# Performance work log

Hardware: AMD Instinct MI355X
Metric: run time of the kernel (lower is better)

The kernel has to match this reference:

```python
import jax, jax.numpy as jnp
import numpy as np

B, N, D = 32, 4096, 256
NC, NTPC, NVPT, NS = 16, 8, 4, 16
NT = NC * NTPC          # 128 type codes
NV = NT * NVPT          # 512 variant codes
THRESH = 0.1            # code_sparsity


def setup_inputs() -> dict:
    key = jax.random.key(0)
    ks = jax.random.split(key, 24)
    rn = lambda k, s, sc=0.02: jax.random.normal(k, s, jnp.float32) * sc
    return {
        "X": jax.random.normal(ks[0], (B, N, D), jnp.float32),
        "positions": jax.random.normal(ks[1], (B, N, D), jnp.float32),
        "mask": jnp.ones((B, N), jnp.bool_),
        "category_codes": rn(ks[2], (NC, D)),
        "type_codes": rn(ks[3], (NT, D)),
        "variant_codes": rn(ks[4], (NV, D)),
        "spatial_codes": rn(ks[5], (NS, D)),
        "log_tau": jnp.zeros((1,), jnp.float32),
        "Wk": rn(ks[6], (D, D)), "bk": jnp.zeros((D,), jnp.float32),
        "Wcat": rn(ks[7], (D, D)), "bcat": jnp.zeros((D,), jnp.float32),
        "Wtype": rn(ks[8], (D, D)), "btype": jnp.zeros((D,), jnp.float32),
        "Wvar": rn(ks[9], (D, D)), "bvar": jnp.zeros((D,), jnp.float32),
        "Wsp": rn(ks[10], (D, D)), "bsp": jnp.zeros((D,), jnp.float32),
        "Wg1": rn(ks[11], (D, 2 * D)), "bg1": jnp.zeros((D,), jnp.float32),
        "Wg2": rn(ks[12], (D, D)), "bg2": jnp.zeros((D,), jnp.float32),
        "Wo": rn(ks[13], (D, D)), "bo": jnp.zeros((D,), jnp.float32),
        "ln_g": jnp.ones((D,), jnp.float32), "ln_b": jnp.zeros((D,), jnp.float32),
        "level_weights": jnp.ones((4,), jnp.float32) / 4.0,
    }


def _sparsify(w, thr):
    w = jnp.where(w > thr, w, 0.0)
    return w / (w.sum(-1, keepdims=True) + 1e-8)


def reference(X, positions, mask, category_codes, type_codes, variant_codes,
              spatial_codes, log_tau, Wk, bk, Wcat, bcat, Wtype, btype,
              Wvar, bvar, Wsp, bsp, Wg1, bg1, Wg2, bg2, Wo, bo, ln_g, ln_b,
              level_weights):
    d = X.shape[-1]
    tau = jnp.clip(jnp.exp(log_tau) + 0.1, 0.1, 2.0)  # (1,)
    mv = jnp.finfo(X.dtype).min / 2
    K = X @ Wk.T + bk  # (B,N,d)

    def level(codes, Wq, bq):
        Q = codes @ Wq.T + bq                                    # (M,d)
        attn = jnp.einsum('md,bnd->bmn', Q, K) / jnp.sqrt(jnp.float32(d))
        attn = jnp.where(mask[:, None, :], attn, mv)
        attn = jnp.clip(attn, -50.0, 50.0)
        G = jnp.nan_to_num(jax.nn.softmax(attn, axis=-1))
        H = jnp.einsum('bmn,bnd->bmd', G, X)                     # (B,M,d)
        w_raw = jnp.linalg.norm(H, axis=-1) / tau                # (B,M)
        return H, w_raw

    # level 0: category
    H_cat, w_cat_raw = level(category_codes, Wcat, bcat)
    w_cat_sparse = _sparsify(jax.nn.softmax(w_cat_raw, -1), THRESH)
    # level 1: type (gated by category)
    H_type, w_type_raw = level(type_codes, Wtype, btype)
    w_type_g = (w_type_raw.reshape(-1, NC, NTPC) * w_cat_sparse[:, :, None]).reshape(-1, NT)
    w_type_sparse = _sparsify(jax.nn.softmax(w_type_g, -1), THRESH / 2)
    # level 2: variant (gated by type)
    H_var, w_var_raw = level(variant_codes, Wvar, bvar)
    w_type_exp = jnp.repeat(w_type_sparse, NVPT, axis=-1)        # (B,NV)
    w_var_sparse = _sparsify(jax.nn.softmax(w_var_raw * w_type_exp, -1), THRESH / 4)
    # spatial (independent)
    H_sp, w_sp_raw = level(spatial_codes, Wsp, bsp)
    w_sp_sparse = _sparsify(jax.nn.softmax(w_sp_raw, -1), THRESH)

    z_cat = jnp.einsum('bm,bmd->bd', w_cat_sparse, H_cat)
    z_type = jnp.einsum('bm,bmd->bd', w_type_sparse, H_type)
    z_var = jnp.einsum('bm,bmd->bd', w_var_sparse, H_var)
    z_sp = jnp.einsum('bm,bmd->bd', w_sp_sparse, H_sp)

    lw = jax.nn.softmax(level_weights)
    z = lw[0] * z_cat + lw[1] * z_type + lw[2] * z_var + lw[3] * z_sp

    # position gate: masked mean-pooled positions -> sigmoid gate
    m = mask.astype(X.dtype)
    pos_pool = (positions * m[:, :, None]).sum(1) / (m.sum(1, keepdims=True) + 1e-8)
    h = jax.nn.gelu(jnp.concatenate([z, pos_pool], -1) @ Wg1.T + bg1, approximate=False)
    gate = jax.nn.sigmoid(h @ Wg2.T + bg2)
    z = z * gate

    # out_proj: Linear + LayerNorm
    y = z @ Wo.T + bo
    mu = y.mean(-1, keepdims=True)
    var = ((y - mu) ** 2).mean(-1, keepdims=True)
    y = (y - mu) / jnp.sqrt(var + 1e-5) * ln_g + ln_b
    return y
```

## Files before the change

### kernel.cpp

```cpp
#include <hip/hip_runtime.h>

typedef unsigned short u16;
typedef short v8s __attribute__((ext_vector_type(8)));
typedef float v4f __attribute__((ext_vector_type(4)));

union U16x8 { uint4 u4; v8s s8; u16 us[8]; };

__device__ __forceinline__ u16 f2bf(float x) {
  unsigned int u = __float_as_uint(x);
  u += 0x7fffu + ((u >> 16) & 1u);
  return (u16)(u >> 16);
}

#define GLOBAL_AS __attribute__((address_space(1)))
#define LDS_AS __attribute__((address_space(3)))
__device__ __forceinline__ void async16(const void* g, void* l) {
  __builtin_amdgcn_global_load_lds((const GLOBAL_AS unsigned int*)g,
                                   (LDS_AS unsigned int*)l, 16, 0, 0);
}

#define BB 32
#define NN 4096
#define DD 256
#define M_TOT 672
#define M_PAD 704
#define MT_PER_B 11

__global__ void kz_zero(float* __restrict__ p, int n) {
  int i = blockIdx.x * 256 + threadIdx.x;
  if (i < n) p[i] = 0.f;
}

__global__ void k0_q(const float* __restrict__ cat, const float* __restrict__ typ,
                     const float* __restrict__ var, const float* __restrict__ spc,
                     const float* __restrict__ Wcat, const float* __restrict__ bcat,
                     const float* __restrict__ Wtype, const float* __restrict__ btype,
                     const float* __restrict__ Wvar, const float* __restrict__ bvar,
                     const float* __restrict__ Wsp, const float* __restrict__ bsp,
                     float* __restrict__ Qall) {
  __shared__ float cl[DD];
  const int m = blockIdx.x, tid = threadIdx.x;
  const float* codes = nullptr; const float* W = nullptr; const float* bia = nullptr; int r = 0;
  if (m < 16)       { codes = cat; r = m;       W = Wcat;  bia = bcat; }
  else if (m < 144) { codes = typ; r = m - 16;  W = Wtype; bia = btype; }
  else if (m < 656) { codes = var; r = m - 144; W = Wvar;  bia = bvar; }
  else if (m < 672) { codes = spc; r = m - 656; W = Wsp;   bia = bsp; }
  cl[tid] = (m < M_TOT) ? codes[r * DD + tid] : 0.f;
  __syncthreads();
  if (m < M_TOT) {
    float acc = bia[tid];
    const float4* w4 = (const float4*)(W + (size_t)tid * DD);
    const float4* c4 = (const float4*)cl;
    #pragma unroll 8
    for (int k = 0; k < 64; ++k) {
      float4 a = c4[k], b = w4[k];
      acc += a.x * b.x + a.y * b.y + a.z * b.z + a.w * b.w;
    }
    Qall[m * DD + tid] = acc;
  } else {
    Qall[m * DD + tid] = 0.f;
  }
}

__global__ void k1_qp(const float* __restrict__ Qall, const float* __restrict__ Wk,
                      const float* __restrict__ bk, u16* __restrict__ Qp,
                      float* __restrict__ qbw) {
  __shared__ float ql[DD];
  __shared__ float red[4];
  const int m = blockIdx.x, tid = threadIdx.x;
  ql[tid] = Qall[m * DD + tid];
  __syncthreads();
  float acc = 0.f;
  for (int j = 0; j < DD; ++j) acc += ql[j] * Wk[(size_t)j * DD + tid];
  Qp[m * DD + tid] = f2bf(acc);
  float p = ql[tid] * bk[tid];
  #pragma unroll
  for (int off = 32; off > 0; off >>= 1) p += __shfl_down(p, off, 64);
  if ((tid & 63) == 0) red[tid >> 6] = p;
  __syncthreads();
  if (tid == 0) qbw[m] = red[0] + red[1] + red[2] + red[3];
}

__global__ void k2_cast(const float* __restrict__ X, u16* __restrict__ Xb,
                        u16* __restrict__ XbT) {
  __shared__ u16 tl[64][72];
  const int n0 = blockIdx.x * 64, d0 = blockIdx.y * 64, b = blockIdx.z;
  const int tid = threadIdx.x;
  const int nl = tid >> 4, d4 = tid & 15;
  #pragma unroll
  for (int rr = 0; rr < 4; ++rr) {
    const int n = n0 + nl + rr * 16;
    float4 v = *(const float4*)(X + ((size_t)b * NN + n) * DD + d0 + d4 * 4);
    ushort4 h;
    h.x = f2bf(v.x); h.y = f2bf(v.y); h.z = f2bf(v.z); h.w = f2bf(v.w);
    *(ushort4*)(Xb + ((size_t)b * NN + n) * DD + d0 +
                (((d4 >> 1) ^ (n & 7)) << 3) + (d4 & 1) * 4) = h;
    *(ushort4*)(&tl[nl + rr * 16][d4 * 4]) = h;
  }
  __syncthreads();
  const int dl = tid >> 4, n4 = tid & 15;
  #pragma unroll
  for (int rr = 0; rr < 4; ++rr) {
    const int d = dl + rr * 16;
    ushort4 h;
    h.x = tl[n4 * 4 + 0][d]; h.y = tl[n4 * 4 + 1][d];
    h.z = tl[n4 * 4 + 2][d]; h.w = tl[n4 * 4 + 3][d];
    *(ushort4*)(XbT + ((size_t)b * DD + d0 + d) * NN + n0 +
                (((n4 >> 1) ^ (dl & 7)) << 3) + (n4 & 1) * 4) = h;
  }
}

__global__ __launch_bounds__(256, 2) void pf_fused(
    const u16* __restrict__ Xb, const u16* __restrict__ XbT,
    const u16* __restrict__ Qp, const float* __restrict__ qbw,
    const unsigned char* __restrict__ mask,
    float* __restrict__ Hws, float* __restrict__ sums, float* __restrict__ nrm) {
  __shared__ u16 sX[64 * 256];
  __shared__ u16 sXT[256 * 64];
  __shared__ u16 sP[64 * 64];

  const int id = blockIdx.x;
  const int orig = (id & 7) * 44 + (id >> 3);
  const int b = orig / MT_PER_B;
  const int m0 = (orig - b * MT_PER_B) * 64;

  const int tid = threadIdx.x;
  const int lane = tid & 63, w = tid >> 6;
  const int q = lane >> 4, c16 = lane & 15;
  const int wmQ = (w >> 1) * 32, wn = (w & 1) * 32;
  const int wd = w * 64;

  v8s aq[2][4][2];
  #pragma unroll
  for (int mi = 0; mi < 2; ++mi) {
    const u16* qrow = Qp + (size_t)(m0 + wmQ + mi * 16 + c16) * DD;
    #pragma unroll
    for (int ks = 0; ks < 4; ++ks)
      #pragma unroll
      for (int kk = 0; kk < 2; ++kk) {
        U16x8 u; u.u4 = *(const uint4*)(qrow + ks * 64 + kk * 32 + q * 8);
        aq[mi][ks][kk] = u.s8;
      }
  }
  float qv[2][4];
  #pragma unroll
  for (int mi = 0; mi < 2; ++mi)
    #pragma unroll
    for (int r = 0; r < 4; ++r)
      qv[mi][r] = qbw[m0 + wmQ + mi * 16 + q * 4 + r];

  v4f hacc[4][4];
  #pragma unroll
  for (int mi = 0; mi < 4; ++mi)
    #pragma unroll
    for (int di = 0; di < 4; ++di) hacc[mi][di] = (v4f){0.f, 0.f, 0.f, 0.f};
  float rs[2][4];
  #pragma unroll
  for (int mi = 0; mi < 2; ++mi)
    #pragma unroll
    for (int r = 0; r < 4; ++r) rs[mi][r] = 0.f;

  const u16* XbB = Xb + (size_t)b * NN * DD;
  const u16* XTB = XbT + (size_t)b * DD * NN;
  const unsigned char* mkB = mask + (size_t)b * NN;

  for (int it = 0; it < 64; ++it) {
    const int n0g = it * 64;
    __syncthreads();
    #pragma unroll
    for (int i = 0; i < 8; ++i) {
      const int c = i * 256 + tid;
      async16(XbB + (size_t)(n0g + (c >> 5)) * DD + (c & 31) * 8, sX + c * 8);
    }
    #pragma unroll
    for (int i = 0; i < 8; ++i) {
      const int c = i * 256 + tid;
      async16(XTB + (size_t)(c >> 3) * NN + n0g + (c & 7) * 8, sXT + c * 8);
    }
    __syncthreads();

    v4f sacc[2][2];
    #pragma unroll
    for (int mi = 0; mi < 2; ++mi)
      #pragma unroll
      for (int ni = 0; ni < 2; ++ni) sacc[mi][ni] = (v4f){0.f, 0.f, 0.f, 0.f};
    #pragma unroll
    for (int ks = 0; ks < 4; ++ks)
      #pragma unroll
      for (int kk = 0; kk < 2; ++kk) {
        v8s bq[2];
        #pragma unroll
        for (int ni = 0; ni < 2; ++ni) {
          const int n = wn + ni * 16 + c16;
          U16x8 u;
          u.u4 = *(const uint4*)(sX + n * 256 + (((ks * 8 + kk * 4 + q) ^ (n & 7)) << 3));
          bq[ni] = u.s8;
        }
        #pragma unroll
        for (int mi = 0; mi < 2; ++mi)
          #pragma unroll
          for (int ni = 0; ni < 2; ++ni)
            sacc[mi][ni] = __builtin_amdgcn_mfma_f32_16x16x32_bf16(
                aq[mi][ks][kk], bq[ni], sacc[mi][ni], 0, 0, 0);
      }

    #pragma unroll
    for (int ni = 0; ni < 2; ++ni) {
      const int nl = wn + ni * 16 + c16;
      const bool mk = mkB[n0g + nl] != 0;
      #pragma unroll
      for (int mi = 0; mi < 2; ++mi)
        #pragma unroll
        for (int r = 0; r < 4; ++r) {
          float s = (sacc[mi][ni][r] + qv[mi][r]) * 0.0625f;
          s = fminf(fmaxf(s, -50.f), 50.f);
          s = mk ? s : -50.f;
          float p = __expf(s);
          rs[mi][r] += p;
          const int ml = wmQ + mi * 16 + q * 4 + r;
          sP[ml * 64 + (nl ^ ((ml & 7) << 3))] = f2bf(p);
        }
    }
    __syncthreads();

    #pragma unroll
    for (int kk = 0; kk < 2; ++kk) {
      v8s pa[4];
      #pragma unroll
      for (int mi = 0; mi < 4; ++mi) {
        const int ml = mi * 16 + c16;
        U16x8 u;
        u.u4 = *(const uint4*)(sP + ml * 64 + ((kk * 32 + q * 8) ^ ((ml & 7) << 3)));
        pa[mi] = u.s8;
      }
      #pragma unroll
      for (int di = 0; di < 4; ++di) {
        const int d = wd + di * 16 + c16;
        U16x8 u;
        u.u4 = *(const uint4*)(sXT + d * 64 + (((kk * 4 + q) ^ (d & 7)) << 3));
        #pragma unroll
        for (int mi = 0; mi < 4; ++mi)
          hacc[mi][di] = __builtin_amdgcn_mfma_f32_16x16x32_bf16(
              pa[mi], u.s8, hacc[mi][di], 0, 0, 0);
      }
    }
  }

  #pragma unroll
  for (int mi = 0; mi < 4; ++mi)
    #pragma unroll
    for (int di = 0; di < 4; ++di)
      #pragma unroll
      for (int r = 0; r < 4; ++r) {
        const int m = m0 + mi * 16 + q * 4 + r;
        Hws[((size_t)b * M_PAD + m) * DD + wd + di * 16 + c16] = hacc[mi][di][r];
      }

  __syncthreads();
  float* fred = (float*)sP;
  #pragma unroll
  for (int mi = 0; mi < 2; ++mi)
    #pragma unroll
    for (int r = 0; r < 4; ++r) {
      float v = rs[mi][r];
      v += __shfl_xor(v, 1, 64);
      v += __shfl_xor(v, 2, 64);
      v += __shfl_xor(v, 4, 64);
      v += __shfl_xor(v, 8, 64);
      if (c16 == 0) fred[(w & 1) * 64 + wmQ + mi * 16 + q * 4 + r] = v;
    }
  #pragma unroll
  for (int mi = 0; mi < 4; ++mi)
    #pragma unroll
    for (int r = 0; r < 4; ++r) {
      float v = 0.f;
      #pragma unroll
      for (int di = 0; di < 4; ++di) {
        float h = hacc[mi][di][r];
        v += h * h;
      }
      v += __shfl_xor(v, 1, 64);
      v += __shfl_xor(v, 2, 64);
      v += __shfl_xor(v, 4, 64);
      v += __shfl_xor(v, 8, 64);
      if (c16 == 0) fred[128 + w * 64 + mi * 16 + q * 4 + r] = v;
    }
  __syncthreads();
  if (tid < 64) {
    const size_t o = (size_t)b * M_PAD + m0 + tid;
    sums[o] = fred[tid] + fred[64 + tid];
    nrm[o] = fred[128 + tid] + fred[192 + tid] + fred[256 + tid] + fred[320 + tid];
  }
}

__global__ void k4_pool(const float* __restrict__ pos, const unsigned char* __restrict__ mask,
                        float* __restrict__ pp, float* __restrict__ cnt) {
  __shared__ float sp[4][256];
  __shared__ float sc[4];
  const int cx = blockIdx.x, b = blockIdx.y, tid = threadIdx.x;
  const int nl = tid >> 6, d4 = tid & 63;
  const int n0 = cx * 256;
  float4 acc = {0.f, 0.f, 0.f, 0.f};
  float c = 0.f;
  for (int i = 0; i < 64; ++i) {
    const int n = n0 + i * 4 + nl;
    const float m = mask[(size_t)b * NN + n] ? 1.f : 0.f;
    c += m;
    float4 v = *(const float4*)(pos + ((size_t)b * NN + n) * DD + d4 * 4);
    acc.x += m * v.x; acc.y += m * v.y; acc.z += m * v.z; acc.w += m * v.w;
  }
  *(float4*)(&sp[nl][d4 * 4]) = acc;
  if (d4 == 0) sc[nl] = c;
  __syncthreads();
  pp[((size_t)b * 16 + cx) * DD + tid] = sp[0][tid] + sp[1][tid] + sp[2][tid] + sp[3][tid];
  if (tid == 0) cnt[b * 16 + cx] = sc[0] + sc[1] + sc[2] + sc[3];
}

__device__ void softmax_sparsify(const float* in, int nn, float* outp, float thr) {
  float mx = -3.4e38f;
  for (int i = 0; i < nn; ++i) mx = fmaxf(mx, in[i]);
  float s = 0.f;
  for (int i = 0; i < nn; ++i) { float e = __expf(in[i] - mx); outp[i] = e; s += e; }
  float s2 = 0.f;
  for (int i = 0; i < nn; ++i) {
    float v = outp[i] / s;
    v = (v > thr) ? v : 0.f;
    outp[i] = v; s2 += v;
  }
  const float inv = 1.f / (s2 + 1e-8f);
  for (int i = 0; i < nn; ++i) outp[i] *= inv;
}

__global__ void k5a_weights(const float* __restrict__ nrm, const float* __restrict__ sums,
                            const float* __restrict__ log_tau,
                            const float* __restrict__ lvlw, float* __restrict__ wbufG) {
  __shared__ float wr[M_TOT];
  __shared__ float wcat[16], wtyp[128], wvar[512], wsp[16], lw[4];
  __shared__ float tmp[128];
  const int b = blockIdx.x, tid = threadIdx.x;
  const float tau = fminf(fmaxf(__expf(log_tau[0]) + 0.1f, 0.1f), 2.0f);
  for (int m = tid; m < M_TOT; m += 256)
    wr[m] = sqrtf(nrm[(size_t)b * M_PAD + m]) / (sums[(size_t)b * M_PAD + m] * tau);
  __syncthreads();
  if (tid == 0) {
    softmax_sparsify(wr, 16, wcat, 0.1f);
    for (int i = 0; i < 128; ++i) tmp[i] = wr[16 + i] * wcat[i >> 3];
    softmax_sparsify(tmp, 128, wtyp, 0.05f);
    for (int i = 0; i < 512; ++i) wvar[i] = wr[144 + i] * wtyp[i >> 2];
    softmax_sparsify(wvar, 512, wvar, 0.025f);
    softmax_sparsify(wr + 656, 16, wsp, 0.1f);
    float mx = fmaxf(fmaxf(lvlw[0], lvlw[1]), fmaxf(lvlw[2], lvlw[3]));
    float s = 0.f;
    for (int i = 0; i < 4; ++i) { lw[i] = __expf(lvlw[i] - mx); s += lw[i]; }
    for (int i = 0; i < 4; ++i) lw[i] /= s;
  }
  __syncthreads();
  for (int m = tid; m < M_TOT; m += 256) {
    float v;
    if (m < 16)       v = lw[0] * wcat[m];
    else if (m < 144) v = lw[1] * wtyp[m - 16];
    else if (m < 656) v = lw[2] * wvar[m - 144];
    else              v = lw[3] * wsp[m - 656];
    wbufG[(size_t)b * M_PAD + m] = v / sums[(size_t)b * M_PAD + m];
  }
}

__global__ void k5b_z(const float* __restrict__ Hws, const float* __restrict__ wbufG,
                      float* __restrict__ zacc) {
  const int mc = blockIdx.x, b = blockIdx.y, tid = threadIdx.x;
  const float* Hb = Hws + (size_t)b * M_PAD * DD;
  const float* wb = wbufG + (size_t)b * M_PAD;
  float acc = 0.f;
  #pragma unroll 4
  for (int i = 0; i < 84; ++i) {
    const int m = mc * 84 + i;
    acc += wb[m] * Hb[(size_t)m * DD + tid];
  }
  atomicAdd(&zacc[(size_t)b * DD + tid], acc);
}

__global__ void k5c_mlp(const float* __restrict__ zacc, const float* __restrict__ pp,
                        const float* __restrict__ cnt,
                        const float* __restrict__ Wg1, const float* __restrict__ bg1,
                        const float* __restrict__ Wg2, const float* __restrict__ bg2,
                        const float* __restrict__ Wo, const float* __restrict__ bo,
                        const float* __restrict__ lng, const float* __restrict__ lnb,
                        float* __restrict__ out) {
  __shared__ float zb[DD], pb[DD], hb[DD], zg[DD];
  __shared__ float red[8];
  const int b = blockIdx.x, tid = threadIdx.x;
  const int lane = tid & 63, w = tid >> 6;

  float p = 0.f, c = 0.f;
  for (int ch = 0; ch < 16; ++ch) {
    p += pp[((size_t)b * 16 + ch) * DD + tid];
    c += cnt[b * 16 + ch];
  }
  zb[tid] = zacc[(size_t)b * DD + tid];
  pb[tid] = p / (c + 1e-8f);
  __syncthreads();

  float h = bg1[tid];
  {
    const float4* w4 = (const float4*)(Wg1 + (size_t)tid * 512);
    const float4* z4 = (const float4*)zb;
    const float4* p4 = (const float4*)pb;
    for (int k = 0; k < 64; ++k) {
      float4 a = z4[k], bb = w4[k];
      h += a.x * bb.x + a.y * bb.y + a.z * bb.z + a.w * bb.w;
    }
    for (int k = 0; k < 64; ++k) {
      float4 a = p4[k], bb = w4[64 + k];
      h += a.x * bb.x + a.y * bb.y + a.z * bb.z + a.w * bb.w;
    }
  }
  h = 0.5f * h * (1.f + erff(h * 0.70710678118654752f));
  hb[tid] = h;
  __syncthreads();

  float g = bg2[tid];
  {
    const float4* w4 = (const float4*)(Wg2 + (size_t)tid * DD);
    const float4* h4 = (const float4*)hb;
    for (int k = 0; k < 64; ++k) {
      float4 a = h4[k], bb = w4[k];
      g += a.x * bb.x + a.y * bb.y + a.z * bb.z + a.w * bb.w;
    }
  }
  g = 1.f / (1.f + __expf(-g));
  zg[tid] = zb[tid] * g;
  __syncthreads();

  float y = bo[tid];
  {
    const float4* w4 = (const float4*)(Wo + (size_t)tid * DD);
    const float4* z4 = (const float4*)zg;
    for (int k = 0; k < 64; ++k) {
      float4 a = z4[k], bb = w4[k];
      y += a.x * bb.x + a.y * bb.y + a.z * bb.z + a.w * bb.w;
    }
  }

  float s = y;
  #pragma unroll
  for (int off = 32; off > 0; off >>= 1) s += __shfl_xor(s, off, 64);
  if (lane == 0) red[w] = s;
  __syncthreads();
  const float mu = (red[0] + red[1] + red[2] + red[3]) * (1.f / 256.f);
  float dv = (y - mu) * (y - mu);
  #pragma unroll
  for (int off = 32; off > 0; off >>= 1) dv += __shfl_xor(dv, off, 64);
  if (lane == 0) red[4 + w] = dv;
  __syncthreads();
  const float var = (red[4] + red[5] + red[6] + red[7]) * (1.f / 256.f);
  out[(size_t)b * DD + tid] = (y - mu) / sqrtf(var + 1e-5f) * lng[tid] + lnb[tid];
}

extern "C" void kernel_launch(void* const* d_in, const int* in_sizes, int n_in,
                              void* d_out, int out_size, void* d_ws, size_t ws_size,
                              hipStream_t stream) {
  const float* X          = (const float*)d_in[0];
  const float* positions  = (const float*)d_in[1];
  const unsigned char* mask = (const unsigned char*)d_in[2];
  const float* cat  = (const float*)d_in[3];
  const float* typ  = (const float*)d_in[4];
  const float* var  = (const float*)d_in[5];
  const float* spc  = (const float*)d_in[6];
  const float* log_tau = (const float*)d_in[7];
  const float* Wk   = (const float*)d_in[8];   const float* bk    = (const float*)d_in[9];
  const float* Wcat = (const float*)d_in[10];  const float* bcat  = (const float*)d_in[11];
  const float* Wtype= (const float*)d_in[12];  const float* btype = (const float*)d_in[13];
  const float* Wvar = (const float*)d_in[14];  const float* bvar  = (const float*)d_in[15];
  const float* Wsp  = (const float*)d_in[16];  const float* bsp   = (const float*)d_in[17];
  const float* Wg1  = (const float*)d_in[18];  const float* bg1   = (const float*)d_in[19];
  const float* Wg2  = (const float*)d_in[20];  const float* bg2   = (const float*)d_in[21];
  const float* Wo   = (const float*)d_in[22];  const float* bo    = (const float*)d_in[23];
  const float* lng  = (const float*)d_in[24];  const float* lnb   = (const float*)d_in[25];
  const float* lvlw = (const float*)d_in[26];

  char* ws = (char*)d_ws;
  size_t off = 0;
  auto alloc = [&](size_t bytes) { size_t o = off; off = (off + bytes + 255) & ~255ULL; return o; };
  const size_t oXb   = alloc((size_t)BB * NN * DD * 2);
  const size_t oXT   = alloc((size_t)BB * DD * NN * 2);
  const size_t oQall = alloc((size_t)M_PAD * DD * 4);
  const size_t oQp   = alloc((size_t)M_PAD * DD * 2);
  const size_t oQb   = alloc((size_t)M_PAD * 4);
  const size_t oSums = alloc((size_t)BB * M_PAD * 4);
  const size_t oNrm  = alloc((size_t)BB * M_PAD * 4);
  const size_t oZac  = alloc((size_t)BB * DD * 4);
  const size_t oWbf  = alloc((size_t)BB * M_PAD * 4);
  const size_t oH    = alloc((size_t)BB * M_PAD * DD * 4);
  const size_t oPP   = alloc((size_t)BB * 16 * DD * 4);
  const size_t oCNT  = alloc((size_t)BB * 16 * 4);

  u16*   Xb   = (u16*)(ws + oXb);
  u16*   XbT  = (u16*)(ws + oXT);
  float* Qall = (float*)(ws + oQall);
  u16*   Qp   = (u16*)(ws + oQp);
  float* qbw  = (float*)(ws + oQb);
  float* sums = (float*)(ws + oSums);
  float* nrm  = (float*)(ws + oNrm);
  float* zacc = (float*)(ws + oZac);
  float* wbfG = (float*)(ws + oWbf);
  float* Hws  = (float*)(ws + oH);
  float* ppw  = (float*)(ws + oPP);
  float* cntw = (float*)(ws + oCNT);

  const int nzero = BB * DD;
  kz_zero<<<(nzero + 255) / 256, 256, 0, stream>>>(zacc, nzero);
  k0_q<<<M_PAD, 256, 0, stream>>>(cat, typ, var, spc, Wcat, bcat, Wtype, btype,
                                  Wvar, bvar, Wsp, bsp, Qall);
  k1_qp<<<M_PAD, 256, 0, stream>>>(Qall, Wk, bk, Qp, qbw);
  k2_cast<<<dim3(64, 4, 32), 256, 0, stream>>>(X, Xb, XbT);
  k4_pool<<<dim3(16, 32), 256, 0, stream>>>(positions, mask, ppw, cntw);
  pf_fused<<<dim3(BB * MT_PER_B), 256, 0, stream>>>(Xb, XbT, Qp, qbw, mask,
                                                    Hws, sums, nrm);
  k5a_weights<<<32, 256, 0, stream>>>(nrm, sums, log_tau, lvlw, wbfG);
  k5b_z<<<dim3(8, 32), 256, 0, stream>>>(Hws, wbfG, zacc);
  k5c_mlp<<<32, 256, 0, stream>>>(zacc, ppw, cntw, Wg1, bg1, Wg2, bg2, Wo, bo,
                                  lng, lnb, (float*)d_out);
}
```

Before: 743.3 us.

## Split the N dimension of the fused attention kernel four ways with a reduce pass

The fused attention-pooling kernel previously launched 352 blocks, each looping over all 4096 tokens, which underfills a 256-CU device at 2 blocks per CU. The change splits the token range into four chunks so 1408 blocks run, writing partial H tiles and partial softmax-free sums to a new workspace. A new reduce kernel adds the four partials in place, computes the row norms, and combines the sums. This works because the attention weights are not normalised per chunk, so the partials add directly. The cost is four times the H write traffic (about 23 MB per split), an extra kernel launch and more re-reads of Q fragments.

```diff
diff --git a/kernel.cpp b/kernel.cpp
--- a/kernel.cpp
+++ b/kernel.cpp
@@ -25,6 +25,8 @@
 #define M_TOT 672
 #define M_PAD 704
 #define MT_PER_B 11
+#define NSPLIT 4
+#define NCHUNK (NN / NSPLIT)
 
 __global__ void kz_zero(float* __restrict__ p, int n) {
   int i = blockIdx.x * 256 + threadIdx.x;
@@ -114,15 +116,18 @@
     const u16* __restrict__ Xb, const u16* __restrict__ XbT,
     const u16* __restrict__ Qp, const float* __restrict__ qbw,
     const unsigned char* __restrict__ mask,
-    float* __restrict__ Hws, float* __restrict__ sums, float* __restrict__ nrm) {
+    float* __restrict__ HP, float* __restrict__ sumsP) {
   __shared__ u16 sX[64 * 256];
   __shared__ u16 sXT[256 * 64];
   __shared__ u16 sP[64 * 64];
 
   const int id = blockIdx.x;
-  const int orig = (id & 7) * 44 + (id >> 3);
-  const int b = orig / MT_PER_B;
-  const int m0 = (orig - b * MT_PER_B) * 64;
+  const int xcd = id & 7, lin = id >> 3;
+  const int ggl = lin / MT_PER_B, k = lin - ggl * MT_PER_B;
+  const int gg = xcd * 16 + ggl;
+  const int b = gg >> 2, split = gg & 3;
+  const int m0 = k * 64;
+  const int ns0 = split * NCHUNK;
 
   const int tid = threadIdx.x;
   const int lane = tid & 63, w = tid >> 6;
@@ -164,8 +169,8 @@
   const u16* XTB = XbT + (size_t)b * DD * NN;
   const unsigned char* mkB = mask + (size_t)b * NN;
 
-  for (int it = 0; it < 64; ++it) {
-    const int n0g = it * 64;
+  for (int it = 0; it < NCHUNK / 64; ++it) {
+    const int n0g = ns0 + it * 64;
     __syncthreads();
     #pragma unroll
     for (int i = 0; i < 8; ++i) {
@@ -246,6 +251,7 @@
     }
   }
 
+  float* HPb = HP + ((size_t)split * BB + b) * M_PAD * DD;
   #pragma unroll
   for (int mi = 0; mi < 4; ++mi)
     #pragma unroll
@@ -253,7 +259,7 @@
       #pragma unroll
       for (int r = 0; r < 4; ++r) {
         const int m = m0 + mi * 16 + q * 4 + r;
-        Hws[((size_t)b * M_PAD + m) * DD + wd + di * 16 + c16] = hacc[mi][di][r];
+        HPb[(size_t)m * DD + wd + di * 16 + c16] = hacc[mi][di][r];
       }
 
   __syncthreads();
@@ -269,27 +275,40 @@
       v += __shfl_xor(v, 8, 64);
       if (c16 == 0) fred[(w & 1) * 64 + wmQ + mi * 16 + q * 4 + r] = v;
     }
-  #pragma unroll
-  for (int mi = 0; mi < 4; ++mi)
-    #pragma unroll
-    for (int r = 0; r < 4; ++r) {
-      float v = 0.f;
-      #pragma unroll
-      for (int di = 0; di < 4; ++di) {
-        float h = hacc[mi][di][r];
-        v += h * h;
-      }
-      v += __shfl_xor(v, 1, 64);
-      v += __shfl_xor(v, 2, 64);
-      v += __shfl_xor(v, 4, 64);
-      v += __shfl_xor(v, 8, 64);
-      if (c16 == 0) fred[128 + w * 64 + mi * 16 + q * 4 + r] = v;
-    }
+  __syncthreads();
+  if (tid < 64) {
+    sumsP[((size_t)split * BB + b) * M_PAD + m0 + tid] = fred[tid] + fred[64 + tid];
+  }
+}
+
+__global__ void khr_reduce(float* __restrict__ HP, const float* __restrict__ sumsP,
+                           float* __restrict__ sums, float* __restrict__ nrm) {
+  __shared__ float red[64][4];
+  const int mt = blockIdx.x, b = blockIdx.y, tid = threadIdx.x;
+  const int lane = tid & 63, w = tid >> 6;
+  const int m0 = mt * 64;
+  const size_t SP = (size_t)BB * M_PAD * DD;
+  float* base = HP + ((size_t)b * M_PAD + m0) * DD;
+  for (int mi = 0; mi < 64; ++mi) {
+    const size_t idx = (size_t)mi * DD + tid;
+    float h = base[idx] + base[idx + SP] + base[idx + 2 * SP] + base[idx + 3 * SP];
+    base[idx] = h;
+    float v = h * h;
+    v += __shfl_xor(v, 1, 64);
+    v += __shfl_xor(v, 2, 64);
+    v += __shfl_xor(v, 4, 64);
+    v += __shfl_xor(v, 8, 64);
+    v += __shfl_xor(v, 16, 64);
+    v += __shfl_xor(v, 32, 64);
+    if (lane == 0) red[mi][w] = v;
+  }
   __syncthreads();
   if (tid < 64) {
     const size_t o = (size_t)b * M_PAD + m0 + tid;
-    sums[o] = fred[tid] + fred[64 + tid];
-    nrm[o] = fred[128 + tid] + fred[192 + tid] + fred[256 + tid] + fred[320 + tid];
+    nrm[o] = red[tid][0] + red[tid][1] + red[tid][2] + red[tid][3];
+    const size_t ss = (size_t)BB * M_PAD;
+    const size_t si = (size_t)b * M_PAD + m0 + tid;
+    sums[o] = sumsP[si] + sumsP[si + ss] + sumsP[si + 2 * ss] + sumsP[si + 3 * ss];
   }
 }
 
@@ -487,10 +506,11 @@
   const size_t oQp   = alloc((size_t)M_PAD * DD * 2);
   const size_t oQb   = alloc((size_t)M_PAD * 4);
   const size_t oSums = alloc((size_t)BB * M_PAD * 4);
+  const size_t oSumsP= alloc((size_t)NSPLIT * BB * M_PAD * 4);
   const size_t oNrm  = alloc((size_t)BB * M_PAD * 4);
   const size_t oZac  = alloc((size_t)BB * DD * 4);
   const size_t oWbf  = alloc((size_t)BB * M_PAD * 4);
-  const size_t oH    = alloc((size_t)BB * M_PAD * DD * 4);
+  const size_t oHP   = alloc((size_t)NSPLIT * BB * M_PAD * DD * 4);
   const size_t oPP   = alloc((size_t)BB * 16 * DD * 4);
   const size_t oCNT  = alloc((size_t)BB * 16 * 4);
 
@@ -500,10 +520,11 @@
   u16*   Qp   = (u16*)(ws + oQp);
   float* qbw  = (float*)(ws + oQb);
   float* sums = (float*)(ws + oSums);
+  float* sumsP= (float*)(ws + oSumsP);
   float* nrm  = (float*)(ws + oNrm);
   float* zacc = (float*)(ws + oZac);
   float* wbfG = (float*)(ws + oWbf);
-  float* Hws  = (float*)(ws + oH);
+  float* HP   = (float*)(ws + oHP);
   float* ppw  = (float*)(ws + oPP);
   float* cntw = (float*)(ws + oCNT);
 
@@ -514,10 +535,11 @@
   k1_qp<<<M_PAD, 256, 0, stream>>>(Qall, Wk, bk, Qp, qbw);
   k2_cast<<<dim3(64, 4, 32), 256, 0, stream>>>(X, Xb, XbT);
   k4_pool<<<dim3(16, 32), 256, 0, stream>>>(positions, mask, ppw, cntw);
-  pf_fused<<<dim3(BB * MT_PER_B), 256, 0, stream>>>(Xb, XbT, Qp, qbw, mask,
-                                                    Hws, sums, nrm);
+  pf_fused<<<dim3(BB * MT_PER_B * NSPLIT), 256, 0, stream>>>(Xb, XbT, Qp, qbw, mask,
+                                                             HP, sumsP);
+  khr_reduce<<<dim3(MT_PER_B, BB), 256, 0, stream>>>(HP, sumsP, sums, nrm);
   k5a_weights<<<32, 256, 0, stream>>>(nrm, sums, log_tau, lvlw, wbfG);
-  k5b_z<<<dim3(8, 32), 256, 0, stream>>>(Hws, wbfG, zacc);
+  k5b_z<<<dim3(8, 32), 256, 0, stream>>>(HP, wbfG, zacc);
   k5c_mlp<<<32, 256, 0, stream>>>(zacc, ppw, cntw, Wg1, bg1, Wg2, bg2, Wo, bo,
                                   lng, lnb, (float*)d_out);
 }
```

Measured after the change: 736.3 us. Within noise of the previous version (-0.9%).
